# Kernel optimization log

Measured on AMD Instinct MI355X. Metric: run time of the kernel, lower is better.

## Reference

```python
import jax, jax.numpy as jnp
import numpy as np

B, T, C, N = 4, 4, 32, 16384
F_OUT = 64
K = 9          # kernel_size
DIL = 1        # dilation
PAD = 4 * DIL  # padding * dilation, as in the torch module


def _unfold1d(a, k, pad, dil):
    """im2col along the last axis. a: [..., N] -> [..., k, N] (stride 1)."""
    ap = jnp.pad(a, [(0, 0)] * (a.ndim - 1) + [(pad, pad)])
    n = a.shape[-1]
    idx = jnp.arange(k)[:, None] * dil + jnp.arange(n)[None, :]  # [k, N]
    return ap[..., idx]


def setup_inputs() -> dict:
    key = jax.random.key(0)
    k1, k2, k3 = jax.random.split(key, 3)
    x = jax.random.normal(k1, (B, T, C, N), dtype=jnp.float32)
    coords = jax.random.normal(k2, (B, T, 3, N), dtype=jnp.float32)
    weight = jax.random.normal(k3, (T, F_OUT, C, K), dtype=jnp.float32) * 0.05
    return {"x": x, "coords": coords, "weight": weight, "sigma": 2}


def reference(x, coords, weight, sigma):
    # im2col windows of features: [B, T, C, K, N]  (channel-major then kernel,
    # matching F.unfold's (C*K, L) layout)
    win = _unfold1d(x, K, PAD, DIL)
    # im2col windows of coords: [B, T, 3, K, N]
    cw = _unfold1d(coords, K, PAD, DIL)
    # subtract center tap (k = K//2)
    diff = cw - cw[:, :, :, K // 2, :][:, :, :, None, :]
    d2 = jnp.sum(diff * diff, axis=2)  # [B, T, K, N]
    # safe sqrt: forward-identical, avoids NaN grads at the zero-distance center
    d = jnp.where(d2 > 0, jnp.sqrt(jnp.where(d2 > 0, d2, 1.0)), 0.0)
    # distance weights, clamped at 0 (torch: dist_weights[dist_weights<0]=0)
    w = jnp.maximum(1.0 - d / sigma, 0.0)  # [B, T, K, N]
    # weight windows; repeat over C in torch == broadcast over C here
    win = win * w[:, :, None, :, :]  # [B, T, C, K, N]
    # batched matmul over flattened (C*K): out[b,t,f,n]
    out = jnp.einsum('btckn,tfck->btfn', win, weight)
    return out
```

## Files before the change

kernel.cpp:

```cpp
#include <hip/hip_runtime.h>
#include <math.h>

#define Bd   4
#define Td   4
#define Cd   32
#define Nd   16384
#define Fd   64
#define Kd   9
#define PADd 4
#define NT   128
#define NROWS (NT + 2*PADd)
#define NCHUNK (NROWS/4)
#define XP    40
#define EPIT  36

typedef __attribute__((ext_vector_type(8))) _Float16 half8;
typedef __attribute__((ext_vector_type(4))) float    float4v;

#define A_WS_BYTES ((size_t)Td * Kd * 4 * 64 * 8 * 2)

#define SM_XT  0
#define SM_WL  10880
#define SM_CS  15488
#define SM_BYTES 18432

union FragU { uint4 u; half8 h; };

__device__ __forceinline__ float sigma_as_float(const void* p) {
    int iv = *(const int*)p;
    if (iv > 0 && iv < 1000000) return (float)iv;
    return __int_as_float(iv);
}

__device__ __forceinline__ unsigned short f32_to_f16_bits(float f) {
    _Float16 h = (_Float16)f;
    return *reinterpret_cast<unsigned short*>(&h);
}

__global__ void prep_weights(const float* __restrict__ w, unsigned short* __restrict__ a) {
    int idx = blockIdx.x * 256 + threadIdx.x;
    if (idx >= Td * Kd * 4 * 64 * 8) return;
    int j    = idx & 7;
    int lane = (idx >> 3) & 63;
    int ft   = (idx >> 9) & 3;
    int k    = (idx >> 11) % Kd;
    int t    = idx / (Kd * 4 * 64 * 8);
    int m = lane & 15, q = lane >> 4;
    int f = ft * 16 + m;
    int c = q * 8 + j;
    float v = w[(((size_t)t * Fd + f) * Cd + c) * Kd + k];
    a[idx] = f32_to_f16_bits(v);
}

__global__ __launch_bounds__(256, 4)
void swconv_mfma4(const float* __restrict__ x,
                  const float* __restrict__ coords,
                  const unsigned short* __restrict__ aw,
                  const void* __restrict__ sigma_p,
                  float* __restrict__ out)
{
    __shared__ __align__(16) unsigned char smem[SM_BYTES];
    unsigned short (*xt)[XP] = (unsigned short (*)[XP])(smem + SM_XT);
    unsigned int (*wlp)[NT]  = (unsigned int (*)[NT])(smem + SM_WL);
    float (*cs)[NROWS]       = (float (*)[NROWS])(smem + SM_CS);

    const int tid  = threadIdx.x;
    const int lane = tid & 63;
    const int wv   = tid >> 6;
    const int tile = blockIdx.x, t = blockIdx.y, b = blockIdx.z;
    const int n0   = tile * NT;
    const float inv_sigma = 1.0f / sigma_as_float(sigma_p);

    const float* xbt = x + (size_t)(b * Td + t) * Cd * Nd;
    #pragma unroll 2
    for (int i = tid; i < Cd * NCHUNK; i += 256) {
        int c  = i / NCHUNK;
        int rq = i - c * NCHUNK;
        int nf = n0 - PADd + rq * 4;
        float4 v = make_float4(0.f, 0.f, 0.f, 0.f);
        if (nf >= 0 && nf < Nd)
            v = *reinterpret_cast<const float4*>(xbt + (size_t)c * Nd + nf);
        int r = rq * 4;
        xt[r + 0][c] = f32_to_f16_bits(v.x);
        xt[r + 1][c] = f32_to_f16_bits(v.y);
        xt[r + 2][c] = f32_to_f16_bits(v.z);
        xt[r + 3][c] = f32_to_f16_bits(v.w);
    }

    const float* cbt = coords + (size_t)(b * Td + t) * 3 * Nd;
    for (int i = tid; i < 3 * NROWS; i += 256) {
        int c = i / NROWS, r = i - c * NROWS;
        int n = n0 - PADd + r;
        cs[c][r] = (n >= 0 && n < Nd) ? cbt[(size_t)c * Nd + n] : 0.0f;
    }

    const int m = lane & 15, q = lane >> 4;
    const unsigned short* Abase = aw + (size_t)t * Kd * 4 * 64 * 8 + (size_t)lane * 8;
    FragU afr[2][4];
    #pragma unroll
    for (int ft = 0; ft < 4; ++ft)
        afr[0][ft].u = *reinterpret_cast<const uint4*>(Abase + (size_t)ft * 512);

    __syncthreads();

    {
        int nl   = wv * 32 + (lane & 31);
        int half = lane >> 5;
        int il   = nl + PADd;
        float c0 = cs[0][il], c1 = cs[1][il], c2 = cs[2][il];
        int k0 = half ? 5 : 0, k1 = half ? Kd : 5;
        #pragma unroll
        for (int k = k0; k < k1; ++k) {
            float d0 = cs[0][nl + k] - c0;
            float d1 = cs[1][nl + k] - c1;
            float d2 = cs[2][nl + k] - c2;
            float s = d0 * d0 + d1 * d1 + d2 * d2;
            float d = (s > 0.0f) ? sqrtf(s) : 0.0f;
            float w = fmaxf(1.0f - d * inv_sigma, 0.0f);
            wlp[k][nl] = (unsigned int)f32_to_f16_bits(w) * 0x00010001u;
        }
    }

    float4v acc[4][2];
    #pragma unroll
    for (int ft = 0; ft < 4; ++ft)
        #pragma unroll
        for (int nt = 0; nt < 2; ++nt)
            acc[ft][nt] = (float4v){0.f, 0.f, 0.f, 0.f};

    for (int k = 0; k < Kd; ++k) {
        const int cur = k & 1;
        if (k + 1 < Kd) {
            #pragma unroll
            for (int ft = 0; ft < 4; ++ft)
                afr[cur ^ 1][ft].u = *reinterpret_cast<const uint4*>(Abase + (size_t)((k + 1) * 4 + ft) * 512);
        }
        #pragma unroll
        for (int nt = 0; nt < 2; ++nt) {
            const int ncol = wv * 32 + nt * 16 + m;
            const int r    = ncol + k;
            FragU xv; xv.u = *reinterpret_cast<const uint4*>(&xt[r][q * 8]);
            unsigned int wp = wlp[k][ncol];
            FragU ww; ww.u = make_uint4(wp, wp, wp, wp);
            half8 bfr = xv.h * ww.h;
            #pragma unroll
            for (int ft = 0; ft < 4; ++ft)
                acc[ft][nt] = __builtin_amdgcn_mfma_f32_16x16x32_f16(afr[cur][ft].h, bfr, acc[ft][nt], 0, 0, 0);
        }
    }

    __syncthreads();
    float (*epi)[EPIT] = (float (*)[EPIT])(smem + (size_t)wv * 32 * EPIT * 4);

    float* ob = out + (size_t)(b * Td + t) * Fd * Nd + n0 + wv * 32;
    #pragma unroll
    for (int fc = 0; fc < 2; ++fc) {
        #pragma unroll
        for (int ft2 = 0; ft2 < 2; ++ft2) {
            const int ft = fc * 2 + ft2;
            #pragma unroll
            for (int nt = 0; nt < 2; ++nt) {
                const int np = nt * 16 + m;
                #pragma unroll
                for (int rr = 0; rr < 4; ++rr)
                    epi[ft2 * 16 + q * 4 + rr][np] = acc[ft][nt][rr];
            }
        }
        #pragma unroll
        for (int inst = 0; inst < 4; ++inst) {
            const int fl = inst * 8 + (lane >> 3);
            const int np = (lane & 7) * 4;
            float4 v = *reinterpret_cast<const float4*>(&epi[fl][np]);
            *reinterpret_cast<float4*>(ob + (size_t)(fc * 32 + fl) * Nd + np) = v;
        }
    }
}

__global__ __launch_bounds__(256, 4)
void swconv_f32_kernel(const float* __restrict__ x,
                       const float* __restrict__ coords,
                       const float* __restrict__ weight,
                       const void*  __restrict__ sigma_p,
                       float* __restrict__ out)
{
    __shared__ float xsf[Cd][NROWS + 1];
    __shared__ float csf[3][NROWS + 1];
    const int tid = threadIdx.x;
    const int tile = blockIdx.x, t = blockIdx.y, b = blockIdx.z;
    const int n0 = tile * NT;
    const float inv_sigma = 1.0f / sigma_as_float(sigma_p);

    const float* xbt = x + (size_t)(b * Td + t) * Cd * Nd;
    for (int idx = tid; idx < Cd * NROWS; idx += 256) {
        int c = idx / NROWS, i = idx - c * NROWS, n = n0 - PADd + i;
        xsf[c][i] = (n >= 0 && n < Nd) ? xbt[(size_t)c * Nd + n] : 0.0f;
    }
    const float* cbt = coords + (size_t)(b * Td + t) * 3 * Nd;
    for (int idx = tid; idx < 3 * NROWS; idx += 256) {
        int c = idx / NROWS, i = idx - c * NROWS, n = n0 - PADd + i;
        csf[c][i] = (n >= 0 && n < Nd) ? cbt[(size_t)c * Nd + n] : 0.0f;
    }
    __syncthreads();
    if (tid >= NT) return;

    float wk[Kd];
    {
        const float c0 = csf[0][tid + PADd], c1 = csf[1][tid + PADd], c2 = csf[2][tid + PADd];
        #pragma unroll
        for (int k = 0; k < Kd; ++k) {
            float d0 = csf[0][tid + k] - c0, d1 = csf[1][tid + k] - c1, d2 = csf[2][tid + k] - c2;
            float s = d0 * d0 + d1 * d1 + d2 * d2;
            float d = (s > 0.0f) ? sqrtf(s) : 0.0f;
            wk[k] = fmaxf(1.0f - d * inv_sigma, 0.0f);
        }
    }
    float accf[Fd];
    #pragma unroll
    for (int f = 0; f < Fd; ++f) accf[f] = 0.0f;
    const float* wt = weight + (size_t)t * Fd * Cd * Kd;
    for (int c = 0; c < Cd; ++c) {
        float xv[Kd];
        #pragma unroll
        for (int k = 0; k < Kd; ++k) xv[k] = xsf[c][tid + k];
        const float* wp = wt + c * Kd;
        #pragma unroll
        for (int k = 0; k < Kd; ++k) {
            float v = xv[k] * wk[k];
            #pragma unroll
            for (int f = 0; f < Fd; ++f)
                accf[f] = fmaf(v, wp[(size_t)f * Cd * Kd + k], accf[f]);
        }
    }
    float* op = out + (size_t)(b * Td + t) * Fd * Nd + n0 + tid;
    #pragma unroll
    for (int f = 0; f < Fd; ++f) op[(size_t)f * Nd] = accf[f];
}

extern "C" void kernel_launch(void* const* d_in, const int* in_sizes, int n_in,
                              void* d_out, int out_size, void* d_ws, size_t ws_size,
                              hipStream_t stream) {
    const float* x      = (const float*)d_in[0];
    const float* coords = (const float*)d_in[1];
    const float* weight = (const float*)d_in[2];
    const void*  sigma  = d_in[3];
    float* out = (float*)d_out;

    if (ws_size >= A_WS_BYTES) {
        unsigned short* aw = (unsigned short*)d_ws;
        prep_weights<<<(Td * Kd * 4 * 64 * 8 + 255) / 256, 256, 0, stream>>>(weight, aw);
        dim3 grid(Nd / NT, Td, Bd);
        swconv_mfma4<<<grid, dim3(256), 0, stream>>>(x, coords, aw, sigma, out);
    } else {
        dim3 grid(Nd / NT, Td, Bd);
        swconv_f32_kernel<<<grid, dim3(256), 0, stream>>>(x, coords, weight, sigma, out);
    }
}
```

Measured before the change: 111.3 us.

## Process two N-tiles per block with double-buffered LDS prefetch

The MFMA kernel now handles two consecutive 128-column tiles per block. The second tile's x and coords global loads are issued into registers before the first tile's MFMA loop, and they land in a second LDS buffer. The epilogue is reworked to stage 16 rows at a time, which lets it share LDS with the first buffer. The intent is to hide global load latency behind compute, at the cost of doubling LDS use, adding register pressure, and halving the grid size (fewer blocks to spread across CUs).

```diff
diff --git a/kernel.cpp b/kernel.cpp
--- a/kernel.cpp
+++ b/kernel.cpp
@@ -19,10 +19,13 @@
 
 #define A_WS_BYTES ((size_t)Td * Kd * 4 * 64 * 8 * 2)
 
-#define SM_XT  0
-#define SM_WL  10880
-#define SM_CS  15488
-#define SM_BYTES 18432
+#define SM_XT0 0
+#define SM_XT1 10880
+#define SM_WL0 21760
+#define SM_WL1 26368
+#define SM_CS0 30976
+#define SM_CS1 32608
+#define SM_BYTES 34240
 
 union FragU { uint4 u; half8 h; };
 
@@ -52,82 +55,90 @@
     a[idx] = f32_to_f16_bits(v);
 }
 
-__global__ __launch_bounds__(256, 4)
-void swconv_mfma4(const float* __restrict__ x,
-                  const float* __restrict__ coords,
-                  const unsigned short* __restrict__ aw,
-                  const void* __restrict__ sigma_p,
-                  float* __restrict__ out)
-{
-    __shared__ __align__(16) unsigned char smem[SM_BYTES];
-    unsigned short (*xt)[XP] = (unsigned short (*)[XP])(smem + SM_XT);
-    unsigned int (*wlp)[NT]  = (unsigned int (*)[NT])(smem + SM_WL);
-    float (*cs)[NROWS]       = (float (*)[NROWS])(smem + SM_CS);
-
-    const int tid  = threadIdx.x;
-    const int lane = tid & 63;
-    const int wv   = tid >> 6;
-    const int tile = blockIdx.x, t = blockIdx.y, b = blockIdx.z;
-    const int n0   = tile * NT;
-    const float inv_sigma = 1.0f / sigma_as_float(sigma_p);
-
-    const float* xbt = x + (size_t)(b * Td + t) * Cd * Nd;
-    #pragma unroll 2
-    for (int i = tid; i < Cd * NCHUNK; i += 256) {
-        int c  = i / NCHUNK;
-        int rq = i - c * NCHUNK;
-        int nf = n0 - PADd + rq * 4;
-        float4 v = make_float4(0.f, 0.f, 0.f, 0.f);
-        if (nf >= 0 && nf < Nd)
-            v = *reinterpret_cast<const float4*>(xbt + (size_t)c * Nd + nf);
-        int r = rq * 4;
-        xt[r + 0][c] = f32_to_f16_bits(v.x);
-        xt[r + 1][c] = f32_to_f16_bits(v.y);
-        xt[r + 2][c] = f32_to_f16_bits(v.z);
-        xt[r + 3][c] = f32_to_f16_bits(v.w);
-    }
-
-    const float* cbt = coords + (size_t)(b * Td + t) * 3 * Nd;
-    for (int i = tid; i < 3 * NROWS; i += 256) {
-        int c = i / NROWS, r = i - c * NROWS;
-        int n = n0 - PADd + r;
-        cs[c][r] = (n >= 0 && n < Nd) ? cbt[(size_t)c * Nd + n] : 0.0f;
-    }
-
-    const int m = lane & 15, q = lane >> 4;
-    const unsigned short* Abase = aw + (size_t)t * Kd * 4 * 64 * 8 + (size_t)lane * 8;
+__device__ __forceinline__ void issue_x(const float* __restrict__ xbt, int n0, int tid, float4 xv[5]) {
+    #pragma unroll
+    for (int i = 0; i < 5; ++i) {
+        int gi = tid + 256 * i;
+        if (i < 4 || tid < Cd * NCHUNK - 1024) {
+            int c = gi / NCHUNK, rq = gi - c * NCHUNK;
+            int nf = n0 - PADd + rq * 4;
+            int nc = min(max(nf, 0), Nd - 4);
+            xv[i] = *reinterpret_cast<const float4*>(xbt + (size_t)c * Nd + nc);
+        }
+    }
+}
+
+__device__ __forceinline__ void write_x(unsigned short (*xt)[XP], int n0, int tid, const float4 xv[5]) {
+    #pragma unroll
+    for (int i = 0; i < 5; ++i) {
+        int gi = tid + 256 * i;
+        if (i < 4 || tid < Cd * NCHUNK - 1024) {
+            int c = gi / NCHUNK, rq = gi - c * NCHUNK;
+            int nf = n0 - PADd + rq * 4;
+            bool ok = (nf >= 0) && (nf <= Nd - 4);
+            float4 v = ok ? xv[i] : make_float4(0.f, 0.f, 0.f, 0.f);
+            int r = rq * 4;
+            xt[r + 0][c] = f32_to_f16_bits(v.x);
+            xt[r + 1][c] = f32_to_f16_bits(v.y);
+            xt[r + 2][c] = f32_to_f16_bits(v.z);
+            xt[r + 3][c] = f32_to_f16_bits(v.w);
+        }
+    }
+}
+
+__device__ __forceinline__ void issue_c(const float* __restrict__ cbt, int n0, int tid, float cv[2]) {
+    #pragma unroll
+    for (int i = 0; i < 2; ++i) {
+        int gi = tid + 256 * i;
+        if (i < 1 || tid < 3 * NROWS - 256) {
+            int c = gi / NROWS, r = gi - c * NROWS;
+            int n = n0 - PADd + r;
+            int nc = min(max(n, 0), Nd - 1);
+            cv[i] = cbt[(size_t)c * Nd + nc];
+        }
+    }
+}
+
+__device__ __forceinline__ void write_c(float (*cs)[NROWS], int n0, int tid, const float cv[2]) {
+    #pragma unroll
+    for (int i = 0; i < 2; ++i) {
+        int gi = tid + 256 * i;
+        if (i < 1 || tid < 3 * NROWS - 256) {
+            int c = gi / NROWS, r = gi - c * NROWS;
+            int n = n0 - PADd + r;
+            bool ok = ((unsigned)n < (unsigned)Nd);
+            cs[c][r] = ok ? cv[i] : 0.0f;
+        }
+    }
+}
+
+__device__ __forceinline__ void wl_comp(const float (*cs)[NROWS], unsigned int (*wlp)[NT],
+                                        int wv, int lane, float inv_sigma) {
+    int nl   = wv * 32 + (lane & 31);
+    int half = lane >> 5;
+    int il   = nl + PADd;
+    float c0 = cs[0][il], c1 = cs[1][il], c2 = cs[2][il];
+    int k0 = half ? 5 : 0, k1 = half ? Kd : 5;
+    #pragma unroll
+    for (int k = k0; k < k1; ++k) {
+        float d0 = cs[0][nl + k] - c0;
+        float d1 = cs[1][nl + k] - c1;
+        float d2 = cs[2][nl + k] - c2;
+        float s = d0 * d0 + d1 * d1 + d2 * d2;
+        float d = (s > 0.0f) ? sqrtf(s) : 0.0f;
+        float w = fmaxf(1.0f - d * inv_sigma, 0.0f);
+        wlp[k][nl] = (unsigned int)f32_to_f16_bits(w) * 0x00010001u;
+    }
+}
+
+__device__ __forceinline__ void kloop(const unsigned char* xt_, const unsigned char* wl_,
+                                      const unsigned short* __restrict__ Abase, const FragU a0[4],
+                                      int wv, int m, int q, float4v acc[4][2]) {
+    const unsigned short (*xt)[XP] = (const unsigned short (*)[XP])xt_;
+    const unsigned int (*wlp)[NT]  = (const unsigned int (*)[NT])wl_;
     FragU afr[2][4];
     #pragma unroll
-    for (int ft = 0; ft < 4; ++ft)
-        afr[0][ft].u = *reinterpret_cast<const uint4*>(Abase + (size_t)ft * 512);
-
-    __syncthreads();
-
-    {
-        int nl   = wv * 32 + (lane & 31);
-        int half = lane >> 5;
-        int il   = nl + PADd;
-        float c0 = cs[0][il], c1 = cs[1][il], c2 = cs[2][il];
-        int k0 = half ? 5 : 0, k1 = half ? Kd : 5;
-        #pragma unroll
-        for (int k = k0; k < k1; ++k) {
-            float d0 = cs[0][nl + k] - c0;
-            float d1 = cs[1][nl + k] - c1;
-            float d2 = cs[2][nl + k] - c2;
-            float s = d0 * d0 + d1 * d1 + d2 * d2;
-            float d = (s > 0.0f) ? sqrtf(s) : 0.0f;
-            float w = fmaxf(1.0f - d * inv_sigma, 0.0f);
-            wlp[k][nl] = (unsigned int)f32_to_f16_bits(w) * 0x00010001u;
-        }
-    }
-
-    float4v acc[4][2];
-    #pragma unroll
-    for (int ft = 0; ft < 4; ++ft)
-        #pragma unroll
-        for (int nt = 0; nt < 2; ++nt)
-            acc[ft][nt] = (float4v){0.f, 0.f, 0.f, 0.f};
-
+    for (int ft = 0; ft < 4; ++ft) afr[0][ft] = a0[ft];
     for (int k = 0; k < Kd; ++k) {
         const int cur = k & 1;
         if (k + 1 < Kd) {
@@ -148,32 +159,99 @@
                 acc[ft][nt] = __builtin_amdgcn_mfma_f32_16x16x32_f16(afr[cur][ft].h, bfr, acc[ft][nt], 0, 0, 0);
         }
     }
-
-    __syncthreads();
-    float (*epi)[EPIT] = (float (*)[EPIT])(smem + (size_t)wv * 32 * EPIT * 4);
-
-    float* ob = out + (size_t)(b * Td + t) * Fd * Nd + n0 + wv * 32;
-    #pragma unroll
-    for (int fc = 0; fc < 2; ++fc) {
-        #pragma unroll
-        for (int ft2 = 0; ft2 < 2; ++ft2) {
-            const int ft = fc * 2 + ft2;
+}
+
+__device__ __forceinline__ void epilogue(float* __restrict__ obt, int n0,
+                                         int wv, int lane, int m, int q,
+                                         unsigned char* smem, const float4v acc[4][2]) {
+    float (*epi)[EPIT] = (float (*)[EPIT])(smem + (size_t)wv * 16 * EPIT * 4);
+    float* ob = obt + n0 + wv * 32;
+    #pragma unroll
+    for (int ft = 0; ft < 4; ++ft) {
+        #pragma unroll
+        for (int nt = 0; nt < 2; ++nt) {
+            const int np = nt * 16 + m;
             #pragma unroll
-            for (int nt = 0; nt < 2; ++nt) {
-                const int np = nt * 16 + m;
-                #pragma unroll
-                for (int rr = 0; rr < 4; ++rr)
-                    epi[ft2 * 16 + q * 4 + rr][np] = acc[ft][nt][rr];
-            }
-        }
-        #pragma unroll
-        for (int inst = 0; inst < 4; ++inst) {
+            for (int rr = 0; rr < 4; ++rr)
+                epi[q * 4 + rr][np] = acc[ft][nt][rr];
+        }
+        #pragma unroll
+        for (int inst = 0; inst < 2; ++inst) {
             const int fl = inst * 8 + (lane >> 3);
             const int np = (lane & 7) * 4;
             float4 v = *reinterpret_cast<const float4*>(&epi[fl][np]);
-            *reinterpret_cast<float4*>(ob + (size_t)(fc * 32 + fl) * Nd + np) = v;
-        }
-    }
+            *reinterpret_cast<float4*>(ob + (size_t)(ft * 16 + fl) * Nd + np) = v;
+        }
+    }
+}
+
+__global__ __launch_bounds__(256, 4)
+void swconv_pipe(const float* __restrict__ x,
+                 const float* __restrict__ coords,
+                 const unsigned short* __restrict__ aw,
+                 const void* __restrict__ sigma_p,
+                 float* __restrict__ out)
+{
+    __shared__ __align__(16) unsigned char smem[SM_BYTES];
+
+    const int tid  = threadIdx.x;
+    const int lane = tid & 63;
+    const int wv   = tid >> 6;
+    const int m    = lane & 15, q = lane >> 4;
+    const int pair = blockIdx.x, t = blockIdx.y, b = blockIdx.z;
+    const int n00  = pair * (2 * NT);
+    const int n01  = n00 + NT;
+    const float inv_sigma = 1.0f / sigma_as_float(sigma_p);
+
+    const float* xbt = x + (size_t)(b * Td + t) * Cd * Nd;
+    const float* cbt = coords + (size_t)(b * Td + t) * 3 * Nd;
+    const unsigned short* Abase = aw + (size_t)t * Kd * 4 * 64 * 8 + (size_t)lane * 8;
+    float* obt = out + (size_t)(b * Td + t) * Fd * Nd;
+
+    float4 xv[5]; float cv[2];
+    FragU a0[4];
+
+    issue_x(xbt, n00, tid, xv);
+    issue_c(cbt, n00, tid, cv);
+    #pragma unroll
+    for (int ft = 0; ft < 4; ++ft)
+        a0[ft].u = *reinterpret_cast<const uint4*>(Abase + (size_t)ft * 512);
+    write_x((unsigned short (*)[XP])(smem + SM_XT0), n00, tid, xv);
+    write_c((float (*)[NROWS])(smem + SM_CS0), n00, tid, cv);
+    __syncthreads();
+    wl_comp((const float (*)[NROWS])(smem + SM_CS0), (unsigned int (*)[NT])(smem + SM_WL0),
+            wv, lane, inv_sigma);
+
+    issue_x(xbt, n01, tid, xv);
+    issue_c(cbt, n01, tid, cv);
+
+    float4v acc[4][2];
+    #pragma unroll
+    for (int ft = 0; ft < 4; ++ft)
+        #pragma unroll
+        for (int nt = 0; nt < 2; ++nt)
+            acc[ft][nt] = (float4v){0.f, 0.f, 0.f, 0.f};
+    kloop(smem + SM_XT0, smem + SM_WL0, Abase, a0, wv, m, q, acc);
+
+    #pragma unroll
+    for (int ft = 0; ft < 4; ++ft)
+        a0[ft].u = *reinterpret_cast<const uint4*>(Abase + (size_t)ft * 512);
+
+    write_x((unsigned short (*)[XP])(smem + SM_XT1), n01, tid, xv);
+    write_c((float (*)[NROWS])(smem + SM_CS1), n01, tid, cv);
+    __syncthreads();
+    wl_comp((const float (*)[NROWS])(smem + SM_CS1), (unsigned int (*)[NT])(smem + SM_WL1),
+            wv, lane, inv_sigma);
+
+    epilogue(obt, n00, wv, lane, m, q, smem, acc);
+
+    #pragma unroll
+    for (int ft = 0; ft < 4; ++ft)
+        #pragma unroll
+        for (int nt = 0; nt < 2; ++nt)
+            acc[ft][nt] = (float4v){0.f, 0.f, 0.f, 0.f};
+    kloop(smem + SM_XT1, smem + SM_WL1, Abase, a0, wv, m, q, acc);
+    epilogue(obt, n01, wv, lane, m, q, smem, acc);
 }
 
 __global__ __launch_bounds__(256, 4)
@@ -219,13 +297,13 @@
     for (int f = 0; f < Fd; ++f) accf[f] = 0.0f;
     const float* wt = weight + (size_t)t * Fd * Cd * Kd;
     for (int c = 0; c < Cd; ++c) {
-        float xv[Kd];
-        #pragma unroll
-        for (int k = 0; k < Kd; ++k) xv[k] = xsf[c][tid + k];
+        float xvv[Kd];
+        #pragma unroll
+        for (int k = 0; k < Kd; ++k) xvv[k] = xsf[c][tid + k];
         const float* wp = wt + c * Kd;
         #pragma unroll
         for (int k = 0; k < Kd; ++k) {
-            float v = xv[k] * wk[k];
+            float v = xvv[k] * wk[k];
             #pragma unroll
             for (int f = 0; f < Fd; ++f)
                 accf[f] = fmaf(v, wp[(size_t)f * Cd * Kd + k], accf[f]);
@@ -248,8 +326,8 @@
     if (ws_size >= A_WS_BYTES) {
         unsigned short* aw = (unsigned short*)d_ws;
         prep_weights<<<(Td * Kd * 4 * 64 * 8 + 255) / 256, 256, 0, stream>>>(weight, aw);
-        dim3 grid(Nd / NT, Td, Bd);
-        swconv_mfma4<<<grid, dim3(256), 0, stream>>>(x, coords, aw, sigma, out);
+        dim3 grid(Nd / (2 * NT), Td, Bd);
+        swconv_pipe<<<grid, dim3(256), 0, stream>>>(x, coords, aw, sigma, out);
     } else {
         dim3 grid(Nd / NT, Td, Bd);
         swconv_f32_kernel<<<grid, dim3(256), 0, stream>>>(x, coords, weight, sigma, out);
```

Measured after the change: 113.2 us. Within noise of the previous version (+1.6%).
